# Optimization experiments

Hardware: AMD Instinct MI355X
Metric: run time of the kernel (lower is better)

## Reference

```python
import jax, jax.numpy as jnp
import numpy as np

WET_MIX = 0.3
FEEDBACK = 0.4
ROOM_SIZE = 0.5
NUM_REFL = 8
NUM_HEADS = 4

# Delay kernel table: int(delay) in {0,1,2,>=3} -> kernel_size {identity,3,5,7}.
# A k-tap kernel with padding k//2 == the same kernel zero-padded to 7 taps with padding 3.
def _gauss7(ks):
    g = np.exp(-np.linspace(-2.0, 2.0, ks) ** 2)
    g = g / g.sum()
    out = np.zeros(7, np.float32)
    s = (7 - ks) // 2
    out[s:s + ks] = g
    return out
_delta = np.zeros(7, np.float32); _delta[3] = 1.0
K_TABLE = jnp.asarray(np.stack([_delta, _gauss7(3), _gauss7(5), _gauss7(7)]))  # [4,7]


def _conv2d(x, w, b, pad):
    y = jax.lax.conv_general_dilated(x, w, (1, 1), [(pad, pad), (pad, pad)],
                                     dimension_numbers=('NCHW', 'OIHW', 'NCHW'))
    return y + b[None, :, None, None]


def _delay_line(x, kern7):
    # vertical depthwise Gaussian blur, same for every (batch, channel) plane
    b, c, h, w = x.shape
    k = kern7.reshape(1, 1, 7, 1)
    y = jax.lax.conv_general_dilated(x.reshape(b * c, 1, h, w), k, (1, 1), [(3, 3), (0, 0)],
                                     dimension_numbers=('NCHW', 'OIHW', 'NCHW'))
    return y.reshape(b, c, h, w)


def _forward(x, refl_w, refl_d, sc_w, sc_b, fb_w, fb_b, d1_w, d1_b, d2_w, d2_b,
             in_proj_w, in_proj_b, out_proj_w, out_proj_b, oc_w, oc_b):
    B, C, H, W = x.shape
    scaled = refl_d * ROOM_SIZE
    kidx = jnp.clip(jnp.floor(scaled).astype(jnp.int32), 0, 3)  # int(delay) detaches grad, as in torch

    wet = jnp.zeros_like(x)
    fb_buf = x * 0.1
    spatial = _conv2d(x, sc_w, sc_b, 1)  # [B,2C,H,W]

    for i in range(NUM_REFL):
        refl = _delay_line(fb_buf, K_TABLE[kidx[i]])
        refl = _conv2d(refl, fb_w, fb_b, 1)
        damp = jax.nn.sigmoid(_conv2d(jax.nn.silu(_conv2d(refl, d1_w, d1_b, 0)), d2_w, d2_b, 0))
        refl = refl * damp
        weight = jax.nn.sigmoid(refl_w[i]) * (0.8 ** i)
        wet = wet + refl * weight
        fb_buf = fb_buf + refl * (FEEDBACK * 0.1)

    # MultiheadAttention over L = H*W tokens, embed_dim=C=4, 4 heads (head_dim=1)
    L = H * W
    hd = C // NUM_HEADS
    wet_flat = wet.reshape(B, C, L).transpose(0, 2, 1)           # [B,L,C]
    qkv = wet_flat @ in_proj_w.T + in_proj_b                     # [B,L,3C]
    q, k, v = jnp.split(qkv, 3, axis=-1)
    def heads(t):
        return t.reshape(B, L, NUM_HEADS, hd).transpose(0, 2, 1, 3)  # [B,H,L,hd]
    q, k, v = heads(q), heads(k), heads(v)
    scores = jnp.einsum('bhqd,bhkd->bhqk', q, k) / np.sqrt(hd).astype(np.float32)
    attn = jax.nn.softmax(scores, axis=-1)
    o = jnp.einsum('bhqk,bhkd->bhqd', attn, v)
    o = o.transpose(0, 2, 1, 3).reshape(B, L, C) @ out_proj_w.T + out_proj_b
    wet2 = o.transpose(0, 2, 1).reshape(B, C, H, W)

    combined = jnp.concatenate([spatial, wet2], axis=1)          # [B,3C,H,W]
    processed_wet = _conv2d(combined, oc_w, oc_b, 0)
    return x * (1.0 - WET_MIX) + processed_wet * WET_MIX


def setup_inputs() -> dict:
    key = jax.random.key(0)
    ks = jax.random.split(key, 16)
    B, C, H, W = 2, 4, 64, 64
    f32 = jnp.float32
    return {
        'x': jax.random.normal(ks[0], (B, C, H, W), f32),
        'refl_w': jax.random.normal(ks[1], (8,), f32) * 0.1,
        'refl_d': jax.random.randint(ks[2], (8,), 1, 16).astype(f32),
        'sc_w': jax.random.normal(ks[3], (2 * C, C, 3, 3), f32) * 0.1,
        'sc_b': jnp.zeros((2 * C,), f32),
        'fb_w': jax.random.normal(ks[4], (C, C, 3, 3), f32) * 0.1,
        'fb_b': jnp.zeros((C,), f32),
        'd1_w': jax.random.normal(ks[5], (C // 2, C, 1, 1), f32) * 0.3,
        'd1_b': jnp.zeros((C // 2,), f32),
        'd2_w': jax.random.normal(ks[6], (C, C // 2, 1, 1), f32) * 0.3,
        'd2_b': jnp.zeros((C,), f32),
        'in_proj_w': jax.random.normal(ks[7], (3 * C, C), f32) * 0.3,
        'in_proj_b': jnp.zeros((3 * C,), f32),
        'out_proj_w': jax.random.normal(ks[8], (C, C), f32) * 0.3,
        'out_proj_b': jnp.zeros((C,), f32),
        'oc_w': jax.random.normal(ks[9], (C, 3 * C, 1, 1), f32) * 0.2,
        'oc_b': jnp.zeros((C,), f32),
    }


def reference(x, refl_w, refl_d, sc_w, sc_b, fb_w, fb_b, d1_w, d1_b, d2_w, d2_b,
              in_proj_w, in_proj_b, out_proj_w, out_proj_b, oc_w, oc_b):
    return _forward(x, refl_w, refl_d, sc_w, sc_b, fb_w, fb_b, d1_w, d1_b, d2_w, d2_b,
                    in_proj_w, in_proj_b, out_proj_w, out_proj_b, oc_w, oc_b)
```

## Files before the change

kernel.cpp:

```cpp
#include <hip/hip_runtime.h>
#include <math.h>


#define ZERO4 make_float4(0.f, 0.f, 0.f, 0.f)

__device__ __forceinline__ float sigf(float v) { return 1.0f / (1.0f + __expf(-v)); }

__device__ __forceinline__ float dppL(float v) {
    return __int_as_float(__builtin_amdgcn_mov_dpp(__float_as_int(v), 0x138, 0xf, 0xf, true));
}
__device__ __forceinline__ float dppR(float v) {
    return __int_as_float(__builtin_amdgcn_mov_dpp(__float_as_int(v), 0x130, 0xf, 0xf, true));
}
__device__ __forceinline__ float4 shL4(float4 v) {
    return make_float4(dppL(v.x), dppL(v.y), dppL(v.z), dppL(v.w));
}
__device__ __forceinline__ float4 shR4(float4 v) {
    return make_float4(dppR(v.x), dppR(v.y), dppR(v.z), dppR(v.w));
}

__device__ __forceinline__ void tapL(float4& a, const float4 t, const float4* w) {
    const float4 w0 = w[0], w1 = w[1], w2 = w[2], w3 = w[3];
    a.x += w0.x * t.x + w1.x * t.y + w2.x * t.z + w3.x * t.w;
    a.y += w0.y * t.x + w1.y * t.y + w2.y * t.z + w3.y * t.w;
    a.z += w0.z * t.x + w1.z * t.y + w2.z * t.z + w3.z * t.w;
    a.w += w0.w * t.x + w1.w * t.y + w2.w * t.z + w3.w * t.w;
}

__global__ __launch_bounds__(1024, 1) void reverb_qkv_kernel(
    const float* __restrict__ x,
    const float* __restrict__ refl_w,
    const float* __restrict__ refl_d,
    const float* __restrict__ fb_w,
    const float* __restrict__ fb_b,
    const float* __restrict__ d1_w,
    const float* __restrict__ d1_b,
    const float* __restrict__ d2_w,
    const float* __restrict__ d2_b,
    const float* __restrict__ ipw,
    const float* __restrict__ ipb,
    float* __restrict__ Qg, float* __restrict__ Kg, float* __restrict__ Vg)
{
    __shared__ float4 P [17 * 64];
    __shared__ float4 BL[17 * 64];
    __shared__ float4 WT[64];
    __shared__ float  GT[3][8];
    __shared__ float  WL[9 * 16];

    const int blk   = blockIdx.x;
    const int batch = blk >> 6;
    const int c0    = blk & 63;
    const int LB    = c0 - 8;
    const int tid   = threadIdx.x;
    const int wy    = tid >> 6;
    const int r     = tid & 63;

    if (tid < 3) {
        const int rr = tid + 1;
        const int ks = 2 * rr + 1;
        const int s  = (7 - ks) >> 1;
        const double step = 4.0 / (double)(ks - 1);
        double g[7]; double sum = 0.0;
        for (int t = 0; t < 7; ++t) {
            if (t < ks) { double u = -2.0 + step * (double)t; g[t] = exp(-u * u); sum += g[t]; }
        }
        for (int t = 0; t < 7; ++t) GT[tid][t] = 0.0f;
        for (int t = 0; t < ks; ++t) GT[tid][s + t] = (float)(g[t] / sum);
    }
    if (tid >= 64 && tid < 64 + 144) {
        const int idx = tid - 64;
        const int oc  = idx / 36;
        const int rem = idx - oc * 36;
        const int ic  = rem / 9;
        const int tp  = rem - ic * 9;
        WL[tp * 16 + ic * 4 + oc] = fb_w[idx];
    }

    for (int idx = tid; idx < 17 * 64; idx += 1024) {
        const int lc  = idx >> 6;
        const int row = idx & 63;
        const int gc  = LB + lc;
        float4 v = ZERO4;
        if (gc >= 0 && gc < 64) {
            const int base = batch * 16384 + row * 64 + gc;
            v.x = 0.1f * x[base];
            v.y = 0.1f * x[base + 4096];
            v.z = 0.1f * x[base + 8192];
            v.w = 0.1f * x[base + 12288];
        }
        P[idx] = v;
    }
    __syncthreads();

    const float4* WL4 = (const float4*)WL;

    double w8 = 1.0;
    for (int j = 0; j < 8; ++j) {
        int kidx = (int)floorf(refl_d[j] * 0.5f);
        kidx = kidx < 0 ? 0 : (kidx > 3 ? 3 : kidx);
        float kv[7];
        #pragma unroll
        for (int u = 0; u < 7; ++u) {
            const float dv = (u == 3) ? 1.0f : 0.0f;
            kv[u] = (kidx == 0) ? dv : GT[kidx - 1][u];
        }
        const float wgt = sigf(refl_w[j]) * (float)w8;

        const int rad = 7 - j;
        const int clo = max(0, c0 - rad);
        const int chi = min(64, c0 + 1 + rad);

        const int lcA   = (clo - 1) - LB;
        const int nBlur = (chi + 1) - (clo - 1);
        for (int t = wy; t < nBlur; t += 16) {
            const int lc = lcA + t;
            const int gc = LB + lc;
            float4 b = ZERO4;
            if (gc >= 0 && gc < 64) {
                const float4 v  = P[lc * 64 + r];
                const float4 l1 = shL4(v),  l2 = shL4(l1), l3 = shL4(l2);
                const float4 r1 = shR4(v),  r2 = shR4(r1), r3 = shR4(r2);
                b.x = kv[0]*l3.x + kv[1]*l2.x + kv[2]*l1.x + kv[3]*v.x
                    + kv[4]*r1.x + kv[5]*r2.x + kv[6]*r3.x;
                b.y = kv[0]*l3.y + kv[1]*l2.y + kv[2]*l1.y + kv[3]*v.y
                    + kv[4]*r1.y + kv[5]*r2.y + kv[6]*r3.y;
                b.z = kv[0]*l3.z + kv[1]*l2.z + kv[2]*l1.z + kv[3]*v.z
                    + kv[4]*r1.z + kv[5]*r2.z + kv[6]*r3.z;
                b.w = kv[0]*l3.w + kv[1]*l2.w + kv[2]*l1.w + kv[3]*v.w
                    + kv[4]*r1.w + kv[5]*r2.w + kv[6]*r3.w;
            }
            BL[lc * 64 + r] = b;
        }
        __syncthreads();

        const int c = clo + wy;
        if (wy < chi - clo) {
            const int lc = c - LB;
            const float4 bm = BL[(lc - 1) * 64 + r];
            const float4 bc = BL[lc * 64 + r];
            const float4 bp = BL[(lc + 1) * 64 + r];

            float4 acc = make_float4(fb_b[0], fb_b[1], fb_b[2], fb_b[3]);
            tapL(acc, shL4(bm), WL4 + 0*4);  tapL(acc, shL4(bc), WL4 + 1*4);  tapL(acc, shL4(bp), WL4 + 2*4);
            tapL(acc, bm,       WL4 + 3*4);  tapL(acc, bc,       WL4 + 4*4);  tapL(acc, bp,       WL4 + 5*4);
            tapL(acc, shR4(bm), WL4 + 6*4);  tapL(acc, shR4(bc), WL4 + 7*4);  tapL(acc, shR4(bp), WL4 + 8*4);

            float4 rr = acc;
            float h0 = d1_b[0] + d1_w[0]*rr.x + d1_w[1]*rr.y + d1_w[2]*rr.z + d1_w[3]*rr.w;
            float h1 = d1_b[1] + d1_w[4]*rr.x + d1_w[5]*rr.y + d1_w[6]*rr.z + d1_w[7]*rr.w;
            h0 = h0 * sigf(h0);
            h1 = h1 * sigf(h1);
            const float d0  = sigf(d2_b[0] + d2_w[0]*h0 + d2_w[1]*h1);
            const float d1v = sigf(d2_b[1] + d2_w[2]*h0 + d2_w[3]*h1);
            const float d2v = sigf(d2_b[2] + d2_w[4]*h0 + d2_w[5]*h1);
            const float d3v = sigf(d2_b[3] + d2_w[6]*h0 + d2_w[7]*h1);
            rr.x *= d0; rr.y *= d1v; rr.z *= d2v; rr.w *= d3v;

            const float4 oldfb = P[lc * 64 + r];
            P[lc * 64 + r] = make_float4(oldfb.x + 0.04f*rr.x, oldfb.y + 0.04f*rr.y,
                                         oldfb.z + 0.04f*rr.z, oldfb.w + 0.04f*rr.w);

            if (c == c0) {
                float4 wv = make_float4(wgt*rr.x, wgt*rr.y, wgt*rr.z, wgt*rr.w);
                if (j > 0) {
                    const float4 old = WT[r];
                    wv.x += old.x; wv.y += old.y; wv.z += old.z; wv.w += old.w;
                }
                WT[r] = wv;
            }
        }
        __syncthreads();
        w8 *= 0.8;
    }

    if (tid < 64) {
        const float4 wv = WT[tid];
        #pragma unroll
        for (int h = 0; h < 4; ++h) {
            const float q = ipb[h]
                + ipw[h*4+0]*wv.x + ipw[h*4+1]*wv.y
                + ipw[h*4+2]*wv.z + ipw[h*4+3]*wv.w;
            const float k = ipb[4+h]
                + ipw[(4+h)*4+0]*wv.x + ipw[(4+h)*4+1]*wv.y
                + ipw[(4+h)*4+2]*wv.z + ipw[(4+h)*4+3]*wv.w;
            const float v = ipb[8+h]
                + ipw[(8+h)*4+0]*wv.x + ipw[(8+h)*4+1]*wv.y
                + ipw[(8+h)*4+2]*wv.z + ipw[(8+h)*4+3]*wv.w;
            const int o = (batch * 4 + h) * 4096 + tid * 64 + c0;
            Qg[o] = q; Kg[o] = k; Vg[o] = v;
        }
    }
}

__global__ __launch_bounds__(512) void attn_kernel(
    const float* __restrict__ Qg, const float* __restrict__ Kg,
    const float* __restrict__ Vg,
    float* __restrict__ PN, float* __restrict__ PD, float* __restrict__ PM)
{
    __shared__ float2 KV[1024];
    __shared__ float  wred[16];
    __shared__ float  pN[4][512], pD[4][512];

    const int bh  = blockIdx.x >> 6;
    const int sub = (blockIdx.x >> 2) & 15;
    const int ks  = blockIdx.x & 3;
    const int tid = threadIdx.x;

    const float* Kp = Kg + bh * 4096 + ks * 1024;
    const float* Vp = Vg + bh * 4096 + ks * 1024;

    float pmax = -3.0e38f, pmin = 3.0e38f;
    #pragma unroll
    for (int t = tid; t < 1024; t += 512) {
        const float kk = Kp[t];
        const float vv = Vp[t];
        KV[t] = make_float2(kk, vv);
        pmax = fmaxf(pmax, kk);
        pmin = fminf(pmin, kk);
    }
    #pragma unroll
    for (int off = 32; off > 0; off >>= 1) {
        pmax = fmaxf(pmax, __shfl_xor(pmax, off, 64));
        pmin = fminf(pmin, __shfl_xor(pmin, off, 64));
    }
    if ((tid & 63) == 0) { wred[tid >> 6] = pmax; wred[8 + (tid >> 6)] = pmin; }
    __syncthreads();
    float kmax = wred[0], kmin = wred[8];
    #pragma unroll
    for (int w = 1; w < 8; ++w) {
        kmax = fmaxf(kmax, wred[w]);
        kmin = fminf(kmin, wred[8 + w]);
    }

    const int ql = tid & 63;
    const int kh = __builtin_amdgcn_readfirstlane(tid >> 6);

    const float L2E = 1.4426950408889634f;
    float q2[4], nm2[4];
    #pragma unroll
    for (int t = 0; t < 4; ++t) {
        const float q = Qg[bh * 4096 + sub * 256 + ql + 64 * t];
        q2[t]  = q * L2E;
        nm2[t] = -(((q >= 0.0f) ? q * kmax : q * kmin) * L2E);
    }

    const float4* KV4 = (const float4*)KV;
    const int base4 = kh * 64;

    float num[4] = {0.f, 0.f, 0.f, 0.f};
    float den[4] = {0.f, 0.f, 0.f, 0.f};
    #pragma unroll 8
    for (int j = 0; j < 64; ++j) {
        const float4 f = KV4[base4 + j];
        #pragma unroll
        for (int t = 0; t < 4; ++t) {
            const float e0 = __builtin_amdgcn_exp2f(__fmaf_rn(q2[t], f.x, nm2[t]));
            den[t] += e0;  num[t] = __fmaf_rn(e0, f.y, num[t]);
            const float e1 = __builtin_amdgcn_exp2f(__fmaf_rn(q2[t], f.z, nm2[t]));
            den[t] += e1;  num[t] = __fmaf_rn(e1, f.w, num[t]);
        }
    }
    #pragma unroll
    for (int t = 0; t < 4; ++t) {
        pN[t][tid] = num[t];
        pD[t][tid] = den[t];
    }
    __syncthreads();
    if (tid < 256) {
        const int which = tid >> 6;
        const int qa    = tid & 63;
        float n = 0.f, d = 0.f;
        #pragma unroll
        for (int w = 0; w < 8; ++w) {
            n += pN[which][w * 64 + qa];
            d += pD[which][w * 64 + qa];
        }
        const int qi = sub * 256 + tid;
        const int o  = bh * 16384 + ks * 4096 + qi;
        PN[o] = n;
        PD[o] = d;
        const float q = Qg[bh * 4096 + qi];
        PM[o] = ((q >= 0.0f) ? q * kmax : q * kmin) * L2E;
    }
}

__global__ __launch_bounds__(128) void final_kernel(
    const float* __restrict__ x,
    const float* __restrict__ sc_w, const float* __restrict__ sc_b,
    const float* __restrict__ opw,  const float* __restrict__ opb,
    const float* __restrict__ ocw,  const float* __restrict__ ocb,
    const float* __restrict__ PN,   const float* __restrict__ PD,
    const float* __restrict__ PM,   float* __restrict__ out)
{
    const int g   = blockIdx.x * 128 + threadIdx.x;
    const int b   = g >> 12;
    const int pix = g & 4095;
    const int y   = pix >> 6;
    const int xc  = pix & 63;

    float xin[4][3][3];
    #pragma unroll
    for (int ic = 0; ic < 4; ++ic)
        #pragma unroll
        for (int ky = 0; ky < 3; ++ky)
            #pragma unroll
            for (int kx = 0; kx < 3; ++kx) {
                const int yy = y + ky - 1, xx = xc + kx - 1;
                xin[ic][ky][kx] = (yy >= 0 && yy < 64 && xx >= 0 && xx < 64)
                                    ? x[(b * 4 + ic) * 4096 + yy * 64 + xx] : 0.f;
            }

    float sp[8];
    #pragma unroll
    for (int oc = 0; oc < 8; ++oc) {
        float a = sc_b[oc];
        #pragma unroll
        for (int ic = 0; ic < 4; ++ic)
            #pragma unroll
            for (int ky = 0; ky < 3; ++ky)
                #pragma unroll
                for (int kx = 0; kx < 3; ++kx)
                    a += sc_w[(oc * 4 + ic) * 9 + ky * 3 + kx] * xin[ic][ky][kx];
        sp[oc] = a;
    }

    float oh[4];
    #pragma unroll
    for (int h = 0; h < 4; ++h) {
        const int bh = b * 4 + h;
        float m2s[4];
        #pragma unroll
        for (int ks = 0; ks < 4; ++ks) m2s[ks] = PM[bh * 16384 + ks * 4096 + pix];
        const float M2 = fmaxf(fmaxf(m2s[0], m2s[1]), fmaxf(m2s[2], m2s[3]));
        float n = 0.f, d = 0.f;
        #pragma unroll
        for (int ks = 0; ks < 4; ++ks) {
            const float s = __builtin_amdgcn_exp2f(m2s[ks] - M2);
            n = __fmaf_rn(PN[bh * 16384 + ks * 4096 + pix], s, n);
            d = __fmaf_rn(PD[bh * 16384 + ks * 4096 + pix], s, d);
        }
        oh[h] = n / d;
    }

    float w2[4];
    #pragma unroll
    for (int c = 0; c < 4; ++c)
        w2[c] = opb[c] + opw[c*4+0]*oh[0] + opw[c*4+1]*oh[1]
                       + opw[c*4+2]*oh[2] + opw[c*4+3]*oh[3];

    #pragma unroll
    for (int c = 0; c < 4; ++c) {
        float a = ocb[c];
        #pragma unroll
        for (int j = 0; j < 8; ++j) a += ocw[c * 12 + j] * sp[j];
        #pragma unroll
        for (int h = 0; h < 4; ++h) a += ocw[c * 12 + 8 + h] * w2[h];
        const int idx = (b * 4 + c) * 4096 + y * 64 + xc;
        out[idx] = 0.7f * x[idx] + 0.3f * a;
    }
}

extern "C" void kernel_launch(void* const* d_in, const int* in_sizes, int n_in,
                              void* d_out, int out_size, void* d_ws, size_t ws_size,
                              hipStream_t stream) {
    const float* x      = (const float*)d_in[0];
    const float* refl_w = (const float*)d_in[1];
    const float* refl_d = (const float*)d_in[2];
    const float* sc_w   = (const float*)d_in[3];
    const float* sc_b   = (const float*)d_in[4];
    const float* fb_w   = (const float*)d_in[5];
    const float* fb_b   = (const float*)d_in[6];
    const float* d1_w   = (const float*)d_in[7];
    const float* d1_b   = (const float*)d_in[8];
    const float* d2_w   = (const float*)d_in[9];
    const float* d2_b   = (const float*)d_in[10];
    const float* ipw    = (const float*)d_in[11];
    const float* ipb    = (const float*)d_in[12];
    const float* opw    = (const float*)d_in[13];
    const float* opb    = (const float*)d_in[14];
    const float* ocw    = (const float*)d_in[15];
    const float* ocb    = (const float*)d_in[16];
    float* out = (float*)d_out;

    float* Q  = (float*)d_ws;
    float* K  = Q + 32768;
    float* V  = K + 32768;
    float* PN = V + 32768;
    float* PD = PN + 131072;
    float* PM = PD + 131072;

    reverb_qkv_kernel<<<dim3(128), dim3(1024), 0, stream>>>(
        x, refl_w, refl_d, fb_w, fb_b, d1_w, d1_b, d2_w, d2_b, ipw, ipb,
        Q, K, V);
    attn_kernel<<<dim3(512), dim3(512), 0, stream>>>(Q, K, V, PN, PD, PM);
    final_kernel<<<dim3(64), dim3(128), 0, stream>>>(
        x, sc_w, sc_b, opw, opb, ocw, ocb, PN, PD, PM, out);
}
```

Measured before the change: 133.4 us.

## Fuse attention and final output stage into one kernel per 32-pixel tile

Merges the attention kernel and the final combine kernel into one kernel. Each block loads the full K/V for all four heads of a batch into padded shared memory, computes attention for 32 pixels, then does the spatial conv, out-projection and output conv in the same block. This removes the PN/PD/PM partial-sum round trip through global memory, the split-K combine and one kernel launch. In exchange every block reloads all 4096 K/V pairs per head, and only 256 blocks with one block per CU (launch bounds 512,1) do the exp-heavy inner loop, so parallelism per query is lower.

New measurement: 128.3 us. -3.8%, faster.

```diff
diff --git a/kernel.cpp b/kernel.cpp
--- a/kernel.cpp
+++ b/kernel.cpp
@@ -192,127 +192,132 @@
     }
 }
 
-__global__ __launch_bounds__(512) void attn_kernel(
-    const float* __restrict__ Qg, const float* __restrict__ Kg,
-    const float* __restrict__ Vg,
-    float* __restrict__ PN, float* __restrict__ PD, float* __restrict__ PM)
-{
-    __shared__ float2 KV[1024];
-    __shared__ float  wred[16];
-    __shared__ float  pN[4][512], pD[4][512];
-
-    const int bh  = blockIdx.x >> 6;
-    const int sub = (blockIdx.x >> 2) & 15;
-    const int ks  = blockIdx.x & 3;
-    const int tid = threadIdx.x;
-
-    const float* Kp = Kg + bh * 4096 + ks * 1024;
-    const float* Vp = Vg + bh * 4096 + ks * 1024;
-
-    float pmax = -3.0e38f, pmin = 3.0e38f;
-    #pragma unroll
-    for (int t = tid; t < 1024; t += 512) {
-        const float kk = Kp[t];
-        const float vv = Vp[t];
-        KV[t] = make_float2(kk, vv);
-        pmax = fmaxf(pmax, kk);
-        pmin = fminf(pmin, kk);
-    }
-    #pragma unroll
-    for (int off = 32; off > 0; off >>= 1) {
-        pmax = fmaxf(pmax, __shfl_xor(pmax, off, 64));
-        pmin = fminf(pmin, __shfl_xor(pmin, off, 64));
-    }
-    if ((tid & 63) == 0) { wred[tid >> 6] = pmax; wred[8 + (tid >> 6)] = pmin; }
-    __syncthreads();
-    float kmax = wred[0], kmin = wred[8];
-    #pragma unroll
-    for (int w = 1; w < 8; ++w) {
-        kmax = fmaxf(kmax, wred[w]);
-        kmin = fminf(kmin, wred[8 + w]);
-    }
-
-    const int ql = tid & 63;
-    const int kh = __builtin_amdgcn_readfirstlane(tid >> 6);
-
-    const float L2E = 1.4426950408889634f;
-    float q2[4], nm2[4];
-    #pragma unroll
-    for (int t = 0; t < 4; ++t) {
-        const float q = Qg[bh * 4096 + sub * 256 + ql + 64 * t];
-        q2[t]  = q * L2E;
-        nm2[t] = -(((q >= 0.0f) ? q * kmax : q * kmin) * L2E);
-    }
-
-    const float4* KV4 = (const float4*)KV;
-    const int base4 = kh * 64;
-
-    float num[4] = {0.f, 0.f, 0.f, 0.f};
-    float den[4] = {0.f, 0.f, 0.f, 0.f};
-    #pragma unroll 8
-    for (int j = 0; j < 64; ++j) {
-        const float4 f = KV4[base4 + j];
-        #pragma unroll
-        for (int t = 0; t < 4; ++t) {
-            const float e0 = __builtin_amdgcn_exp2f(__fmaf_rn(q2[t], f.x, nm2[t]));
-            den[t] += e0;  num[t] = __fmaf_rn(e0, f.y, num[t]);
-            const float e1 = __builtin_amdgcn_exp2f(__fmaf_rn(q2[t], f.z, nm2[t]));
-            den[t] += e1;  num[t] = __fmaf_rn(e1, f.w, num[t]);
-        }
-    }
-    #pragma unroll
-    for (int t = 0; t < 4; ++t) {
-        pN[t][tid] = num[t];
-        pD[t][tid] = den[t];
-    }
-    __syncthreads();
-    if (tid < 256) {
-        const int which = tid >> 6;
-        const int qa    = tid & 63;
-        float n = 0.f, d = 0.f;
-        #pragma unroll
-        for (int w = 0; w < 8; ++w) {
-            n += pN[which][w * 64 + qa];
-            d += pD[which][w * 64 + qa];
-        }
-        const int qi = sub * 256 + tid;
-        const int o  = bh * 16384 + ks * 4096 + qi;
-        PN[o] = n;
-        PD[o] = d;
-        const float q = Qg[bh * 4096 + qi];
-        PM[o] = ((q >= 0.0f) ? q * kmax : q * kmin) * L2E;
-    }
-}
-
-__global__ __launch_bounds__(128) void final_kernel(
+#define KV_CS 258
+#define KV_HS (16 * KV_CS)
+
+__global__ __launch_bounds__(512, 1) void attn_final_kernel(
     const float* __restrict__ x,
     const float* __restrict__ sc_w, const float* __restrict__ sc_b,
     const float* __restrict__ opw,  const float* __restrict__ opb,
     const float* __restrict__ ocw,  const float* __restrict__ ocb,
-    const float* __restrict__ PN,   const float* __restrict__ PD,
-    const float* __restrict__ PM,   float* __restrict__ out)
+    const float* __restrict__ Qg,   const float* __restrict__ Kg,
+    const float* __restrict__ Vg,   float* __restrict__ out)
 {
-    const int g   = blockIdx.x * 128 + threadIdx.x;
-    const int b   = g >> 12;
-    const int pix = g & 4095;
-    const int y   = pix >> 6;
-    const int xc  = pix & 63;
-
-    float xin[4][3][3];
-    #pragma unroll
-    for (int ic = 0; ic < 4; ++ic)
-        #pragma unroll
-        for (int ky = 0; ky < 3; ++ky)
-            #pragma unroll
-            for (int kx = 0; kx < 3; ++kx) {
-                const int yy = y + ky - 1, xx = xc + kx - 1;
-                xin[ic][ky][kx] = (yy >= 0 && yy < 64 && xx >= 0 && xx < 64)
-                                    ? x[(b * 4 + ic) * 4096 + yy * 64 + xx] : 0.f;
-            }
-
-    float sp[8];
-    #pragma unroll
-    for (int oc = 0; oc < 8; ++oc) {
+    __shared__ float2 KV[4 * KV_HS];
+    __shared__ float  XH[4][3][36];
+    __shared__ float2 PND[4][2][32];
+    __shared__ float2 KRED[4][2];
+    __shared__ float  OH[32][4];
+    __shared__ float  W2[32][4];
+    __shared__ float  SP[8][32];
+
+    const int blk = blockIdx.x;
+    const int b   = blk >> 7;
+    const int rem = blk & 127;
+    const int y0  = rem >> 1;
+    const int x0  = (rem & 1) << 5;
+    const int tid = threadIdx.x;
+
+    {
+        const int h = tid >> 7;
+        const int i = tid & 127;
+        const float* Kp = Kg + (b * 4 + h) * 4096;
+        const float* Vp = Vg + (b * 4 + h) * 4096;
+        float kmx = -3.0e38f, kmn = 3.0e38f;
+        #pragma unroll
+        for (int m = 0; m < 32; ++m) {
+            const int j  = i + m * 128;
+            const float kk = Kp[j];
+            const float vv = Vp[j];
+            KV[h * KV_HS + (j >> 8) * KV_CS + (j & 255)] = make_float2(kk, vv);
+            kmx = fmaxf(kmx, kk);
+            kmn = fminf(kmn, kk);
+        }
+        #pragma unroll
+        for (int off = 32; off > 0; off >>= 1) {
+            kmx = fmaxf(kmx, __shfl_xor(kmx, off, 64));
+            kmn = fminf(kmn, __shfl_xor(kmn, off, 64));
+        }
+        if ((tid & 63) == 0) KRED[h][(tid >> 6) & 1] = make_float2(kmx, kmn);
+    }
+    if (tid < 408) {
+        const int ic = tid / 102;
+        const int r2 = tid - ic * 102;
+        const int ry = r2 / 34;
+        const int cc = r2 - ry * 34;
+        const int gy = y0 + ry - 1;
+        const int gx = x0 + cc - 1;
+        XH[ic][ry][cc] = (gy >= 0 && gy < 64 && gx >= 0 && gx < 64)
+                          ? x[(b * 4 + ic) * 4096 + gy * 64 + gx] : 0.0f;
+    }
+    __syncthreads();
+
+    {
+        const int wv   = tid >> 6;
+        const int lane = tid & 63;
+        const int h    = wv >> 1;
+        const int kh   = wv & 1;
+        const int pxg  = lane & 7;
+        const int ks2  = lane >> 3;
+
+        const float2 kr0 = KRED[h][0], kr1 = KRED[h][1];
+        const float kmax = fmaxf(kr0.x, kr1.x);
+        const float kmin = fminf(kr0.y, kr1.y);
+
+        const float L2E = 1.4426950408889634f;
+        const float4 qv = *(const float4*)(Qg + (b * 4 + h) * 4096
+                                           + y0 * 64 + x0 + pxg * 4);
+        float q2[4], nm2[4];
+        {
+            const float qs[4] = {qv.x, qv.y, qv.z, qv.w};
+            #pragma unroll
+            for (int t = 0; t < 4; ++t) {
+                q2[t]  = qs[t] * L2E;
+                nm2[t] = -(((qs[t] >= 0.0f) ? qs[t] * kmax : qs[t] * kmin) * L2E);
+            }
+        }
+
+        const int c0 = kh * 8 + ks2;
+        const float4* KV4 = (const float4*)(KV + h * KV_HS + c0 * KV_CS);
+
+        float num[4] = {0.f, 0.f, 0.f, 0.f};
+        float den[4] = {0.f, 0.f, 0.f, 0.f};
+        #pragma unroll 8
+        for (int jj = 0; jj < 128; ++jj) {
+            const float4 f = KV4[jj];
+            #pragma unroll
+            for (int t = 0; t < 4; ++t) {
+                const float e0 = __builtin_amdgcn_exp2f(__fmaf_rn(q2[t], f.x, nm2[t]));
+                den[t] += e0;  num[t] = __fmaf_rn(e0, f.y, num[t]);
+                const float e1 = __builtin_amdgcn_exp2f(__fmaf_rn(q2[t], f.z, nm2[t]));
+                den[t] += e1;  num[t] = __fmaf_rn(e1, f.w, num[t]);
+            }
+        }
+        #pragma unroll
+        for (int off = 8; off <= 32; off <<= 1) {
+            #pragma unroll
+            for (int t = 0; t < 4; ++t) {
+                num[t] += __shfl_xor(num[t], off, 64);
+                den[t] += __shfl_xor(den[t], off, 64);
+            }
+        }
+        if (ks2 == 0) {
+            #pragma unroll
+            for (int t = 0; t < 4; ++t)
+                PND[h][kh][pxg * 4 + t] = make_float2(num[t], den[t]);
+        }
+    }
+    __syncthreads();
+
+    if (tid < 128) {
+        const int px = tid & 31, hh = tid >> 5;
+        const float2 a = PND[hh][0][px], c = PND[hh][1][px];
+        OH[px][hh] = (a.x + c.x) / (a.y + c.y);
+    }
+    __syncthreads();
+
+    if (tid < 256) {
+        const int px = tid & 31, oc = tid >> 5;
         float a = sc_b[oc];
         #pragma unroll
         for (int ic = 0; ic < 4; ++ic)
@@ -320,43 +325,26 @@
             for (int ky = 0; ky < 3; ++ky)
                 #pragma unroll
                 for (int kx = 0; kx < 3; ++kx)
-                    a += sc_w[(oc * 4 + ic) * 9 + ky * 3 + kx] * xin[ic][ky][kx];
-        sp[oc] = a;
-    }
-
-    float oh[4];
-    #pragma unroll
-    for (int h = 0; h < 4; ++h) {
-        const int bh = b * 4 + h;
-        float m2s[4];
-        #pragma unroll
-        for (int ks = 0; ks < 4; ++ks) m2s[ks] = PM[bh * 16384 + ks * 4096 + pix];
-        const float M2 = fmaxf(fmaxf(m2s[0], m2s[1]), fmaxf(m2s[2], m2s[3]));
-        float n = 0.f, d = 0.f;
-        #pragma unroll
-        for (int ks = 0; ks < 4; ++ks) {
-            const float s = __builtin_amdgcn_exp2f(m2s[ks] - M2);
-            n = __fmaf_rn(PN[bh * 16384 + ks * 4096 + pix], s, n);
-            d = __fmaf_rn(PD[bh * 16384 + ks * 4096 + pix], s, d);
-        }
-        oh[h] = n / d;
-    }
-
-    float w2[4];
-    #pragma unroll
-    for (int c = 0; c < 4; ++c)
-        w2[c] = opb[c] + opw[c*4+0]*oh[0] + opw[c*4+1]*oh[1]
-                       + opw[c*4+2]*oh[2] + opw[c*4+3]*oh[3];
-
-    #pragma unroll
-    for (int c = 0; c < 4; ++c) {
+                    a += sc_w[(oc * 4 + ic) * 9 + ky * 3 + kx] * XH[ic][ky][px + kx];
+        SP[oc][px] = a;
+    } else if (tid < 384) {
+        const int t2 = tid - 256;
+        const int px = t2 & 31, hh = t2 >> 5;
+        W2[px][hh] = opb[hh]
+                   + opw[hh*4+0]*OH[px][0] + opw[hh*4+1]*OH[px][1]
+                   + opw[hh*4+2]*OH[px][2] + opw[hh*4+3]*OH[px][3];
+    }
+    __syncthreads();
+
+    if (tid < 128) {
+        const int px = tid & 31, c = tid >> 5;
         float a = ocb[c];
         #pragma unroll
-        for (int j = 0; j < 8; ++j) a += ocw[c * 12 + j] * sp[j];
-        #pragma unroll
-        for (int h = 0; h < 4; ++h) a += ocw[c * 12 + 8 + h] * w2[h];
-        const int idx = (b * 4 + c) * 4096 + y * 64 + xc;
-        out[idx] = 0.7f * x[idx] + 0.3f * a;
+        for (int j = 0; j < 8; ++j)  a += ocw[c * 12 + j] * SP[j][px];
+        #pragma unroll
+        for (int hh = 0; hh < 4; ++hh) a += ocw[c * 12 + 8 + hh] * W2[px][hh];
+        const int idx = (b * 4 + c) * 4096 + y0 * 64 + x0 + px;
+        out[idx] = 0.7f * XH[c][1][px + 1] + 0.3f * a;
     }
 }
 
@@ -382,17 +370,13 @@
     const float* ocb    = (const float*)d_in[16];
     float* out = (float*)d_out;
 
-    float* Q  = (float*)d_ws;
-    float* K  = Q + 32768;
-    float* V  = K + 32768;
-    float* PN = V + 32768;
-    float* PD = PN + 131072;
-    float* PM = PD + 131072;
+    float* Q = (float*)d_ws;
+    float* K = Q + 32768;
+    float* V = K + 32768;
 
     reverb_qkv_kernel<<<dim3(128), dim3(1024), 0, stream>>>(
         x, refl_w, refl_d, fb_w, fb_b, d1_w, d1_b, d2_w, d2_b, ipw, ipb,
         Q, K, V);
-    attn_kernel<<<dim3(512), dim3(512), 0, stream>>>(Q, K, V, PN, PD, PM);
-    final_kernel<<<dim3(64), dim3(128), 0, stream>>>(
-        x, sc_w, sc_b, opw, opb, ocw, ocb, PN, PD, PM, out);
-}
+    attn_final_kernel<<<dim3(256), dim3(512), 0, stream>>>(
+        x, sc_w, sc_b, opw, opb, ocw, ocb, Q, K, V, out);
+}
```
